# Optimization experiments

Hardware: AMD Instinct MI355X
Metric: run time of the kernel (lower is better)

The kernel has to match this reference:

```python
import jax, jax.numpy as jnp
import numpy as np

B, T, C = 2, 2048, 2048
NH, NKV = 16, 4
HD = C // NH  # 128


def _rope(x, cos, sin):
    d = x.shape[-1] // 2
    x1, x2 = x[..., :d], x[..., d:]
    return jnp.concatenate([x1 * cos + x2 * sin, -x1 * sin + x2 * cos], axis=-1)


def _rmsnorm(x):
    eps = jnp.finfo(x.dtype).eps
    return x * jax.lax.rsqrt(jnp.mean(jnp.square(x), axis=-1, keepdims=True) + eps)


def setup_inputs() -> dict:
    key = jax.random.key(0)
    ks = jax.random.split(key, 7)
    s = 0.02
    return {
        "x": jax.random.normal(ks[0], (B, T, C), jnp.float32),
        "cos": jax.random.normal(ks[1], (1, T, 1, HD // 2), jnp.float32),
        "sin": jax.random.normal(ks[2], (1, T, 1, HD // 2), jnp.float32),
        "wq": jax.random.normal(ks[3], (C, NH * HD), jnp.float32) * s,
        "wk": jax.random.normal(ks[4], (C, NKV * HD), jnp.float32) * s,
        "wv": jax.random.normal(ks[5], (C, NKV * HD), jnp.float32) * s,
        "wo": jax.random.normal(ks[6], (C, C), jnp.float32) * s,
    }


def reference(x, cos, sin, wq, wk, wv, wo):
    q = (x @ wq).reshape(B, T, NH, HD)
    k = (x @ wk).reshape(B, T, NKV, HD)
    v = (x @ wv).reshape(B, T, NKV, HD)
    q = _rmsnorm(_rope(q, cos, sin))
    k = _rmsnorm(_rope(k, cos, sin))
    # [B, H, T, D]
    q = q.transpose(0, 2, 1, 3)
    k = k.transpose(0, 2, 1, 3)
    v = v.transpose(0, 2, 1, 3)
    rep = NH // NKV
    k = jnp.repeat(k, rep, axis=1)
    v = jnp.repeat(v, rep, axis=1)
    scale = 1.0 / jnp.sqrt(jnp.float32(HD))
    scores = jnp.einsum("bhqd,bhkd->bhqk", q, k) * scale
    causal = jnp.tril(jnp.ones((T, T), bool))
    scores = jnp.where(causal, scores, jnp.finfo(scores.dtype).min)
    attn = jax.nn.softmax(scores, axis=-1)
    y = jnp.einsum("bhqk,bhkd->bhqd", attn, v)
    y = y.transpose(0, 2, 1, 3).reshape(B, T, C)
    return y @ wo
```

## Files before the change

kernel.cpp:

```cpp
#include <hip/hip_runtime.h>
#include <hip/hip_bf16.h>
#include <cstdint>

typedef unsigned short u16;
typedef __bf16 bf16x8 __attribute__((ext_vector_type(8)));
typedef float f32x4 __attribute__((ext_vector_type(4)));
typedef unsigned short u16x4 __attribute__((ext_vector_type(4)));
typedef unsigned uint2v __attribute__((ext_vector_type(2)));

#define B_ 2
#define T_ 2048
#define C_ 2048
#define NH_ 16
#define NKV_ 4
#define HD_ 128
#define K2_ 0.12752004650581538f

__device__ __forceinline__ u16 f2bf(float f) {
    unsigned u = __builtin_bit_cast(unsigned, f);
    unsigned r = u + 0x7FFFu + ((u >> 16) & 1u);
    return (u16)(r >> 16);
}

__device__ __forceinline__ float bf2f(u16 v) {
    unsigned u = ((unsigned)v) << 16;
    return __builtin_bit_cast(float, u);
}

__device__ __forceinline__ unsigned cvtpk(float a, float b) {
    unsigned r;
    asm("v_cvt_pk_bf16_f32 %0, %1, %2" : "=v"(r) : "v"(a), "v"(b));
    return r;
}

__device__ __forceinline__ void gl16(const void* g, void* l) {
    auto gp = reinterpret_cast<const __attribute__((address_space(1))) unsigned*>(
        reinterpret_cast<uintptr_t>(g));
    auto lp = reinterpret_cast<__attribute__((address_space(3))) unsigned*>(
        reinterpret_cast<uintptr_t>(l));
    __builtin_amdgcn_global_load_lds(gp, lp, 16, 0, 0);
}

__global__ void transpose_conv(const float* __restrict__ in, u16* __restrict__ out, int N) {
    __shared__ float tile[32][33];
    int n0 = blockIdx.x * 32, k0 = blockIdx.y * 32;
    int tx = threadIdx.x, ty = threadIdx.y;
#pragma unroll
    for (int i = 0; i < 4; ++i)
        tile[ty * 4 + i][tx] = in[(size_t)(k0 + ty * 4 + i) * N + n0 + tx];
    __syncthreads();
#pragma unroll
    for (int i = 0; i < 4; ++i)
        out[(size_t)(n0 + ty * 4 + i) * 2048 + k0 + tx] = f2bf(tile[tx][ty * 4 + i]);
}

__global__ void convert4(const float4* __restrict__ in, u16* __restrict__ out) {
    int i = blockIdx.x * 256 + threadIdx.x;
    float4 v = in[i];
    u16x4 o;
    o[0] = f2bf(v.x); o[1] = f2bf(v.y); o[2] = f2bf(v.z); o[3] = f2bf(v.w);
    ((u16x4*)out)[i] = o;
}

__global__ __launch_bounds__(256, 2) void gemm_bf16(const u16* __restrict__ A,
                                                    const u16* __restrict__ BT,
                                                    float* __restrict__ C, int N, int K) {
    __shared__ __align__(16) u16 As[2][128 * 64];
    __shared__ __align__(16) u16 Bs[2][128 * 64];
    int nwg = gridDim.x * gridDim.y;
    int bid = blockIdx.y * gridDim.x + blockIdx.x;
    int nb = (bid & 7) * (nwg >> 3) + (bid >> 3);
    int bx = nb % gridDim.x, by = nb / gridDim.x;

    int t = threadIdx.x;
    int w = t >> 6, l = t & 63;
    int wr = w >> 1, wc = w & 1;
    int lg = l >> 4, lr = l & 15;
    int m0 = by * 128, n0 = bx * 128;
    f32x4 acc[4][4] = {};

    size_t goff[4];
#pragma unroll
    for (int i = 0; i < 4; ++i) {
        int g = t + i * 256;
        goff[i] = (size_t)(g >> 3) * K * 2 + (size_t)(((g & 7) ^ ((g >> 3) & 7)) * 16);
    }
    const char* Ab = (const char*)A + (size_t)m0 * K * 2;
    const char* Bb = (const char*)BT + (size_t)n0 * K * 2;

    auto stage = [&](int kt, int buf) {
        char* Ad = (char*)As[buf] + t * 16;
        char* Bd = (char*)Bs[buf] + t * 16;
#pragma unroll
        for (int i = 0; i < 4; ++i) {
            gl16(Ab + (size_t)kt * 2 + goff[i], Ad + i * 4096);
            gl16(Bb + (size_t)kt * 2 + goff[i], Bd + i * 4096);
        }
    };

    stage(0, 0);
    int nk = K >> 6;
    for (int ki = 0; ki < nk; ++ki) {
        asm volatile("s_waitcnt vmcnt(0)" ::: "memory");
        __builtin_amdgcn_s_barrier();
        __builtin_amdgcn_sched_barrier(0);
        int cur = ki & 1;
        if (ki + 1 < nk) stage((ki + 1) * 64, cur ^ 1);
#pragma unroll
        for (int kk = 0; kk < 2; ++kk) {
            bf16x8 af[4], bfr[4];
#pragma unroll
            for (int m = 0; m < 4; ++m)
                af[m] = *(const bf16x8*)&As[cur][(wr * 64 + m * 16 + lr) * 64 +
                                                (((kk * 4 + lg) ^ (lr & 7)) * 8)];
#pragma unroll
            for (int n = 0; n < 4; ++n)
                bfr[n] = *(const bf16x8*)&Bs[cur][(wc * 64 + n * 16 + lr) * 64 +
                                                 (((kk * 4 + lg) ^ (lr & 7)) * 8)];
#pragma unroll
            for (int m = 0; m < 4; ++m)
#pragma unroll
                for (int n = 0; n < 4; ++n)
                    acc[m][n] = __builtin_amdgcn_mfma_f32_16x16x32_bf16(af[m], bfr[n], acc[m][n], 0, 0, 0);
        }
    }
#pragma unroll
    for (int m = 0; m < 4; ++m) {
        int row = m0 + wr * 64 + m * 16 + lg * 4;
#pragma unroll
        for (int n = 0; n < 4; ++n) {
            int col = n0 + wc * 64 + n * 16 + lr;
            float* Cp = C + (size_t)row * N + col;
#pragma unroll
            for (int r = 0; r < 4; ++r)
                Cp[(size_t)r * N] = acc[m][n][r];
        }
    }
}

__global__ __launch_bounds__(256, 2) void gemm_bf16o(const u16* __restrict__ A,
                                                     const u16* __restrict__ BT,
                                                     u16* __restrict__ C, int N, int K) {
    __shared__ __align__(16) u16 As[2][128 * 64];
    __shared__ __align__(16) u16 Bs[2][128 * 64];
    int nwg = gridDim.x * gridDim.y;
    int bid = blockIdx.y * gridDim.x + blockIdx.x;
    int nb = (bid & 7) * (nwg >> 3) + (bid >> 3);
    int bx = nb % gridDim.x, by = nb / gridDim.x;

    int t = threadIdx.x;
    int w = t >> 6, l = t & 63;
    int wr = w >> 1, wc = w & 1;
    int lg = l >> 4, lr = l & 15;
    int m0 = by * 128, n0 = bx * 128;
    f32x4 acc[4][4] = {};

    size_t goff[4];
#pragma unroll
    for (int i = 0; i < 4; ++i) {
        int g = t + i * 256;
        goff[i] = (size_t)(g >> 3) * K * 2 + (size_t)(((g & 7) ^ ((g >> 3) & 7)) * 16);
    }
    const char* Ab = (const char*)A + (size_t)m0 * K * 2;
    const char* Bb = (const char*)BT + (size_t)n0 * K * 2;

    auto stage = [&](int kt, int buf) {
        char* Ad = (char*)As[buf] + t * 16;
        char* Bd = (char*)Bs[buf] + t * 16;
#pragma unroll
        for (int i = 0; i < 4; ++i) {
            gl16(Ab + (size_t)kt * 2 + goff[i], Ad + i * 4096);
            gl16(Bb + (size_t)kt * 2 + goff[i], Bd + i * 4096);
        }
    };

    stage(0, 0);
    int nk = K >> 6;
    for (int ki = 0; ki < nk; ++ki) {
        asm volatile("s_waitcnt vmcnt(0)" ::: "memory");
        __builtin_amdgcn_s_barrier();
        __builtin_amdgcn_sched_barrier(0);
        int cur = ki & 1;
        if (ki + 1 < nk) stage((ki + 1) * 64, cur ^ 1);
#pragma unroll
        for (int kk = 0; kk < 2; ++kk) {
            bf16x8 af[4], bfr[4];
#pragma unroll
            for (int m = 0; m < 4; ++m)
                af[m] = *(const bf16x8*)&As[cur][(wr * 64 + m * 16 + lr) * 64 +
                                                (((kk * 4 + lg) ^ (lr & 7)) * 8)];
#pragma unroll
            for (int n = 0; n < 4; ++n)
                bfr[n] = *(const bf16x8*)&Bs[cur][(wc * 64 + n * 16 + lr) * 64 +
                                                 (((kk * 4 + lg) ^ (lr & 7)) * 8)];
#pragma unroll
            for (int m = 0; m < 4; ++m)
#pragma unroll
                for (int n = 0; n < 4; ++n)
                    acc[m][n] = __builtin_amdgcn_mfma_f32_16x16x32_bf16(af[m], bfr[n], acc[m][n], 0, 0, 0);
        }
    }
#pragma unroll
    for (int m = 0; m < 4; ++m) {
        int row = m0 + wr * 64 + m * 16 + lg * 4;
#pragma unroll
        for (int n = 0; n < 4; ++n) {
            int col = n0 + wc * 64 + n * 16 + lr;
            u16* Cp = C + (size_t)row * N + col;
#pragma unroll
            for (int r = 0; r < 4; ++r)
                Cp[(size_t)r * N] = f2bf(acc[m][n][r]);
        }
    }
}

__global__ void rope_rms(const u16* __restrict__ qkv, const float* __restrict__ cs,
                         const float* __restrict__ sn, u16* __restrict__ qh,
                         u16* __restrict__ kh) {
    int task = blockIdx.x * 4 + (threadIdx.x >> 6);
    int l = threadIdx.x & 63;
    const u16* in;
    u16* out;
    int tpos;
    float post = 1.0f;
    if (task < 65536) {
        int row = task >> 4, h = task & 15;
        in = qkv + (size_t)row * 3072 + h * 128;
        int b = row >> 11; tpos = row & 2047;
        out = qh + ((size_t)(b * NH_ + h) * T_ + tpos) * HD_;
        post = K2_;
    } else {
        int t2 = task - 65536;
        int row = t2 >> 2, h = t2 & 3;
        in = qkv + (size_t)row * 3072 + 2048 + h * 128;
        int b = row >> 11; tpos = row & 2047;
        out = kh + ((size_t)(b * NKV_ + h) * T_ + tpos) * HD_;
    }
    float x1 = bf2f(in[l]), x2 = bf2f(in[l + 64]);
    float c = cs[tpos * 64 + l], s = sn[tpos * 64 + l];
    float o1 = x1 * c + x2 * s;
    float o2 = -x1 * s + x2 * c;
    float ss = o1 * o1 + o2 * o2;
#pragma unroll
    for (int m = 1; m < 64; m <<= 1) ss += __shfl_xor(ss, m);
    float r = rsqrtf(ss * (1.0f / 128.0f) + 1.1920929e-07f) * post;
    out[l] = f2bf(o1 * r);
    out[l + 64] = f2bf(o2 * r);
}

__global__ void transpose_v(const u16* __restrict__ qkv, u16* __restrict__ vt) {
    __shared__ u16 tile[32][34];
    int t0 = blockIdx.x * 32;
    int d0 = blockIdx.y * 32;
    int bk = blockIdx.z;
    int b = bk >> 2, kvh = bk & 3;
    int tx = threadIdx.x, ty = threadIdx.y;
#pragma unroll
    for (int i = 0; i < 4; ++i)
        tile[ty * 4 + i][tx] =
            qkv[(size_t)(b * 2048 + t0 + ty * 4 + i) * 3072 + 2560 + kvh * 128 + d0 + tx];
    __syncthreads();
#pragma unroll
    for (int i = 0; i < 4; ++i)
        vt[((size_t)bk * 128 + d0 + ty * 4 + i) * 2048 + t0 + tx] = tile[tx][ty * 4 + i];
}

__global__ __launch_bounds__(256, 2) void attn(const u16* __restrict__ Q,
                                               const u16* __restrict__ Kk,
                                               const u16* __restrict__ V,
                                               u16* __restrict__ Y) {
    extern __shared__ __align__(16) u16 sm[];
    u16* Ks = sm;
    u16* Vs = sm + 16384;
    u16* Pb = sm + 32768;

    int bid = blockIdx.x;
    int xcd = bid & 7;
    int b = xcd >> 2, kvh = xcd & 3;
    int q = bid >> 3;
    int j = (q < 32) ? (63 - q) : (q - 32);
    int NN = (j >> 1) + 1;
    int t = threadIdx.x;
    int w = t >> 6, l = t & 63;
    int lg = l >> 4, lr = l & 15;
    int h = kvh * 4 + w;
    int qw = j * 32;

    const u16* Qp = Q + (size_t)(b * NH_ + h) * T_ * HD_;
    const u16* Kp = Kk + (size_t)(b * NKV_ + kvh) * T_ * HD_;
    const u16* Vp = V + (size_t)(b * NKV_ + kvh) * HD_ * T_;
    u16* Yp = Y + (size_t)(b * T_) * 2048 + h * HD_;
    u16* Pw = Pb + w * 1024;

    size_t koff[4], voff[4];
#pragma unroll
    for (int i = 0; i < 4; ++i) {
        int g = t + i * 256;
        koff[i] = (size_t)(g >> 4) * 256 + (size_t)(((g & 15) ^ ((g >> 4) & 15)) * 16);
        voff[i] = (size_t)(g >> 3) * (T_ * 2) + (size_t)(((g & 7) ^ ((g >> 3) & 7)) * 16);
    }
    auto stage = [&](int kv0, int buf) {
        const char* Kb = (const char*)Kp + (size_t)kv0 * 256;
        const char* Vb = (const char*)Vp + (size_t)kv0 * 2;
        char* Kd = (char*)Ks + buf * 16384 + t * 16;
        char* Vd = (char*)Vs + buf * 16384 + t * 16;
#pragma unroll
        for (int i = 0; i < 4; ++i) {
            gl16(Kb + koff[i], Kd + i * 4096);
            gl16(Vb + voff[i], Vd + i * 4096);
        }
    };

    bf16x8 aq[2][4];
#pragma unroll
    for (int qf = 0; qf < 2; ++qf)
#pragma unroll
        for (int ch = 0; ch < 4; ++ch)
            aq[qf][ch] = *(const bf16x8*)(Qp + (size_t)(qw + qf * 16 + lr) * HD_ + ch * 32 + lg * 8);

    f32x4 acc[2][8] = {};
    float m2[2] = {-1e30f, -1e30f};
    float lp_[2] = {0.0f, 0.0f};

    stage(0, 0);

    for (int gi = 0; gi < NN; ++gi) {
        asm volatile("s_waitcnt vmcnt(0)" ::: "memory");
        __builtin_amdgcn_s_barrier();
        __builtin_amdgcn_sched_barrier(0);
        int cur = gi & 1;
        if (gi + 1 < NN) stage((gi + 1) * 64, cur ^ 1);
        int kv0 = gi * 64;
        int kbase = cur * 8192;

        f32x4 sc[2][4] = {};
        __builtin_amdgcn_s_setprio(1);
#pragma unroll
        for (int ch = 0; ch < 4; ++ch)
#pragma unroll
            for (int kf = 0; kf < 4; ++kf) {
                bf16x8 bk = *(const bf16x8*)&Ks[kbase + (kf * 16 + lr) * 128 + (((ch * 4 + lg) ^ lr) * 8)];
                sc[0][kf] = __builtin_amdgcn_mfma_f32_16x16x32_bf16(bk, aq[0][ch], sc[0][kf], 0, 0, 0);
                sc[1][kf] = __builtin_amdgcn_mfma_f32_16x16x32_bf16(bk, aq[1][ch], sc[1][kf], 0, 0, 0);
            }
        __builtin_amdgcn_s_setprio(0);

        if (kv0 + 63 > qw) {
#pragma unroll
            for (int qf = 0; qf < 2; ++qf) {
                int qrow = qw + qf * 16 + lr;
#pragma unroll
                for (int kf = 0; kf < 4; ++kf)
#pragma unroll
                    for (int r = 0; r < 4; ++r) {
                        int key = kv0 + kf * 16 + 4 * lg + r;
                        if (key > qrow) sc[qf][kf][r] = -1e38f;
                    }
            }
        }
        float mx[2];
#pragma unroll
        for (int qf = 0; qf < 2; ++qf) {
            float m = sc[qf][0][0];
#pragma unroll
            for (int kf = 0; kf < 4; ++kf)
#pragma unroll
                for (int r = 0; r < 4; ++r) m = fmaxf(m, sc[qf][kf][r]);
            m = fmaxf(m, __shfl_xor(m, 16));
            m = fmaxf(m, __shfl_xor(m, 32));
            mx[qf] = m;
        }
        bool upd = (mx[0] > m2[0] + 8.0f) || (mx[1] > m2[1] + 8.0f);
        if (__any(upd)) {
#pragma unroll
            for (int qf = 0; qf < 2; ++qf) {
                float mn = fmaxf(m2[qf], mx[qf]);
                float rs = exp2f(m2[qf] - mn);
                m2[qf] = mn;
                lp_[qf] *= rs;
                float rs4[4];
#pragma unroll
                for (int r = 0; r < 4; ++r) rs4[r] = __shfl(rs, 4 * lg + r, 16);
#pragma unroll
                for (int oc = 0; oc < 8; ++oc)
#pragma unroll
                    for (int r = 0; r < 4; ++r) acc[qf][oc][r] *= rs4[r];
            }
        }
        bf16x8 ap[2][2];
#pragma unroll
        for (int kk = 0; kk < 2; ++kk) {
#pragma unroll
            for (int qf = 0; qf < 2; ++qf) {
                float ps = 0.0f;
#pragma unroll
                for (int kfl = 0; kfl < 2; ++kfl) {
                    int kf = kk * 2 + kfl;
                    float p0 = exp2f(sc[qf][kf][0] - m2[qf]);
                    float p1 = exp2f(sc[qf][kf][1] - m2[qf]);
                    float p2 = exp2f(sc[qf][kf][2] - m2[qf]);
                    float p3 = exp2f(sc[qf][kf][3] - m2[qf]);
                    ps += (p0 + p1) + (p2 + p3);
                    uint2v pk;
                    pk[0] = cvtpk(p0, p1);
                    pk[1] = cvtpk(p2, p3);
                    int g = 2 * kfl + (lg >> 1);
                    *(uint2v*)&Pw[(qf * 16 + lr) * 32 + ((g ^ (lr & 3)) * 8) + (lg & 1) * 4] = pk;
                }
                lp_[qf] += ps;
            }
#pragma unroll
            for (int qf = 0; qf < 2; ++qf)
                ap[qf][kk] = *(const bf16x8*)&Pw[(qf * 16 + lr) * 32 + ((lg ^ (lr & 3)) * 8)];
        }
        __builtin_amdgcn_s_setprio(1);
#pragma unroll
        for (int oc = 0; oc < 8; ++oc)
#pragma unroll
            for (int kk = 0; kk < 2; ++kk) {
                bf16x8 bv = *(const bf16x8*)&Vs[kbase + (oc * 16 + lr) * 64 +
                                                (((kk * 4 + lg) ^ (lr & 7)) * 8)];
                acc[0][oc] = __builtin_amdgcn_mfma_f32_16x16x32_bf16(ap[0][kk], bv, acc[0][oc], 0, 0, 0);
                acc[1][oc] = __builtin_amdgcn_mfma_f32_16x16x32_bf16(ap[1][kk], bv, acc[1][oc], 0, 0, 0);
            }
        __builtin_amdgcn_s_setprio(0);
    }
#pragma unroll
    for (int qf = 0; qf < 2; ++qf) {
        float lt = lp_[qf];
        lt += __shfl_xor(lt, 16);
        lt += __shfl_xor(lt, 32);
        float inv = 1.0f / lt;
        float inv4[4];
#pragma unroll
        for (int r = 0; r < 4; ++r) inv4[r] = __shfl(inv, 4 * lg + r, 16);
#pragma unroll
        for (int oc = 0; oc < 8; ++oc)
#pragma unroll
            for (int r = 0; r < 4; ++r)
                Yp[(size_t)(qw + qf * 16 + 4 * lg + r) * 2048 + oc * 16 + lr] =
                    f2bf(acc[qf][oc][r] * inv4[r]);
    }
}

extern "C" void kernel_launch(void* const* d_in, const int* in_sizes, int n_in,
                              void* d_out, int out_size, void* d_ws, size_t ws_size,
                              hipStream_t stream) {
    const float* x    = (const float*)d_in[0];
    const float* cosT = (const float*)d_in[1];
    const float* sinT = (const float*)d_in[2];
    const float* wq   = (const float*)d_in[3];
    const float* wk   = (const float*)d_in[4];
    const float* wv   = (const float*)d_in[5];
    const float* wo   = (const float*)d_in[6];
    float* out = (float*)d_out;

    char* ws = (char*)d_ws;
    u16*   wqkvT = (u16*)(ws);
    u16*   woT   = (u16*)(ws + 12582912);
    u16*   xb    = (u16*)(ws + 20971520);
    u16*   qkv   = (u16*)(ws + 37748736);
    u16*   qh    = (u16*)(ws + 88080384);
    u16*   kh    = (u16*)(ws + 104857600);
    u16*   vt    = (u16*)(ws + 109051904);
    u16*   y     = xb;

    hipFuncSetAttribute(reinterpret_cast<const void*>(&attn),
                        hipFuncAttributeMaxDynamicSharedMemorySize, 73728);

    transpose_conv<<<dim3(64, 64), dim3(32, 8), 0, stream>>>(wq, wqkvT, 2048);
    transpose_conv<<<dim3(16, 64), dim3(32, 8), 0, stream>>>(wk, wqkvT + (size_t)2048 * 2048, 512);
    transpose_conv<<<dim3(16, 64), dim3(32, 8), 0, stream>>>(wv, wqkvT + (size_t)2560 * 2048, 512);
    transpose_conv<<<dim3(64, 64), dim3(32, 8), 0, stream>>>(wo, woT, 2048);
    convert4<<<8192, 256, 0, stream>>>((const float4*)x, xb);

    gemm_bf16o<<<dim3(24, 32), 256, 0, stream>>>(xb, wqkvT, qkv, 3072, 2048);

    rope_rms<<<20480, 256, 0, stream>>>(qkv, cosT, sinT, qh, kh);
    transpose_v<<<dim3(64, 4, 8), dim3(32, 8), 0, stream>>>(qkv, vt);

    attn<<<512, 256, 73728, stream>>>(qh, kh, vt, y);

    gemm_bf16<<<dim3(16, 32), 256, 0, stream>>>(y, woT, out, 2048, 2048);
}
```

Measured before the change: 203.8 us.

## Single-buffer V tile in attention, prefetch only K, shrink LDS footprint

The attention loop now double-buffers only the K tile. The V tile gets a single buffer, loaded at the start of each iteration and waited on with a partial vmcnt plus a barrier before the PV matmul. The per-wave P scratch is halved by reusing one 16-row slab for both query fragments, which cuts dynamic LDS from 72KB to 52KB. The V load latency is now hidden only by the QK and softmax work in the same iteration. The change also adds an extra block-wide barrier per iteration and a dummy K prefetch on the last iteration.

Result: no change. 202.0 us (-0.9%).

```diff
diff --git a/kernel.cpp b/kernel.cpp
--- a/kernel.cpp
+++ b/kernel.cpp
@@ -272,7 +272,7 @@
     extern __shared__ __align__(16) u16 sm[];
     u16* Ks = sm;
     u16* Vs = sm + 16384;
-    u16* Pb = sm + 32768;
+    u16* Pb = sm + 24576;
 
     int bid = blockIdx.x;
     int xcd = bid & 7;
@@ -290,7 +290,7 @@
     const u16* Kp = Kk + (size_t)(b * NKV_ + kvh) * T_ * HD_;
     const u16* Vp = V + (size_t)(b * NKV_ + kvh) * HD_ * T_;
     u16* Yp = Y + (size_t)(b * T_) * 2048 + h * HD_;
-    u16* Pw = Pb + w * 1024;
+    u16* Pw = Pb + w * 512;
 
     size_t koff[4], voff[4];
 #pragma unroll
@@ -299,16 +299,17 @@
         koff[i] = (size_t)(g >> 4) * 256 + (size_t)(((g & 15) ^ ((g >> 4) & 15)) * 16);
         voff[i] = (size_t)(g >> 3) * (T_ * 2) + (size_t)(((g & 7) ^ ((g >> 3) & 7)) * 16);
     }
-    auto stage = [&](int kv0, int buf) {
+    auto stageK = [&](int kv0, int buf) {
         const char* Kb = (const char*)Kp + (size_t)kv0 * 256;
+        char* Kd = (char*)Ks + buf * 16384 + t * 16;
+#pragma unroll
+        for (int i = 0; i < 4; ++i) gl16(Kb + koff[i], Kd + i * 4096);
+    };
+    auto stageV = [&](int kv0) {
         const char* Vb = (const char*)Vp + (size_t)kv0 * 2;
-        char* Kd = (char*)Ks + buf * 16384 + t * 16;
-        char* Vd = (char*)Vs + buf * 16384 + t * 16;
-#pragma unroll
-        for (int i = 0; i < 4; ++i) {
-            gl16(Kb + koff[i], Kd + i * 4096);
-            gl16(Vb + voff[i], Vd + i * 4096);
-        }
+        char* Vd = (char*)Vs + t * 16;
+#pragma unroll
+        for (int i = 0; i < 4; ++i) gl16(Vb + voff[i], Vd + i * 4096);
     };
 
     bf16x8 aq[2][4];
@@ -322,15 +323,19 @@
     float m2[2] = {-1e30f, -1e30f};
     float lp_[2] = {0.0f, 0.0f};
 
-    stage(0, 0);
+    stageK(0, 0);
 
     for (int gi = 0; gi < NN; ++gi) {
         asm volatile("s_waitcnt vmcnt(0)" ::: "memory");
         __builtin_amdgcn_s_barrier();
         __builtin_amdgcn_sched_barrier(0);
         int cur = gi & 1;
-        if (gi + 1 < NN) stage((gi + 1) * 64, cur ^ 1);
         int kv0 = gi * 64;
+        stageV(kv0);
+        __builtin_amdgcn_sched_barrier(0);
+        int gn = (gi + 1 < NN) ? gi + 1 : 0;
+        stageK(gn * 64, cur ^ 1);
+        __builtin_amdgcn_sched_barrier(0);
         int kbase = cur * 8192;
 
         f32x4 sc[2][4] = {};
@@ -405,26 +410,29 @@
                     pk[0] = cvtpk(p0, p1);
                     pk[1] = cvtpk(p2, p3);
                     int g = 2 * kfl + (lg >> 1);
-                    *(uint2v*)&Pw[(qf * 16 + lr) * 32 + ((g ^ (lr & 3)) * 8) + (lg & 1) * 4] = pk;
+                    *(uint2v*)&Pw[lr * 32 + ((g ^ (lr & 3)) * 8) + (lg & 1) * 4] = pk;
                 }
                 lp_[qf] += ps;
+                ap[qf][kk] = *(const bf16x8*)&Pw[lr * 32 + ((lg ^ (lr & 3)) * 8)];
             }
-#pragma unroll
-            for (int qf = 0; qf < 2; ++qf)
-                ap[qf][kk] = *(const bf16x8*)&Pw[(qf * 16 + lr) * 32 + ((lg ^ (lr & 3)) * 8)];
-        }
+        }
+        asm volatile("s_waitcnt vmcnt(4)" ::: "memory");
+        __builtin_amdgcn_s_barrier();
+        __builtin_amdgcn_sched_barrier(0);
+
         __builtin_amdgcn_s_setprio(1);
 #pragma unroll
         for (int oc = 0; oc < 8; ++oc)
 #pragma unroll
             for (int kk = 0; kk < 2; ++kk) {
-                bf16x8 bv = *(const bf16x8*)&Vs[kbase + (oc * 16 + lr) * 64 +
+                bf16x8 bv = *(const bf16x8*)&Vs[(oc * 16 + lr) * 64 +
                                                 (((kk * 4 + lg) ^ (lr & 7)) * 8)];
                 acc[0][oc] = __builtin_amdgcn_mfma_f32_16x16x32_bf16(ap[0][kk], bv, acc[0][oc], 0, 0, 0);
                 acc[1][oc] = __builtin_amdgcn_mfma_f32_16x16x32_bf16(ap[1][kk], bv, acc[1][oc], 0, 0, 0);
             }
         __builtin_amdgcn_s_setprio(0);
     }
+    asm volatile("s_waitcnt vmcnt(0)" ::: "memory");
 #pragma unroll
     for (int qf = 0; qf < 2; ++qf) {
         float lt = lp_[qf];
@@ -466,7 +474,7 @@
     u16*   y     = xb;
 
     hipFuncSetAttribute(reinterpret_cast<const void*>(&attn),
-                        hipFuncAttributeMaxDynamicSharedMemorySize, 73728);
+                        hipFuncAttributeMaxDynamicSharedMemorySize, 53248);
 
     transpose_conv<<<dim3(64, 64), dim3(32, 8), 0, stream>>>(wq, wqkvT, 2048);
     transpose_conv<<<dim3(16, 64), dim3(32, 8), 0, stream>>>(wk, wqkvT + (size_t)2048 * 2048, 512);
@@ -479,7 +487,7 @@
     rope_rms<<<20480, 256, 0, stream>>>(qkv, cosT, sinT, qh, kh);
     transpose_v<<<dim3(64, 4, 8), dim3(32, 8), 0, stream>>>(qkv, vt);
 
-    attn<<<512, 256, 73728, stream>>>(qh, kh, vt, y);
+    attn<<<512, 256, 53248, stream>>>(qh, kh, vt, y);
 
     gemm_bf16<<<dim3(16, 32), 256, 0, stream>>>(y, woT, out, 2048, 2048);
 }
```
